# Kernel optimization log

Hardware: AMD Instinct MI355X
Metric: run time of the kernel (lower is better)

## Reference

```python
import jax, jax.numpy as jnp
import numpy as np
from jax import lax

FEAT_STRIDE = 16
PRE_NMS_TOP_N = 6000   # cfg['TEST'].RPN_PRE_NMS_TOP_N
POST_NMS_TOP_N = 300   # cfg['TEST'].RPN_POST_NMS_TOP_N
NMS_THRESH = 0.7       # cfg['TEST'].RPN_NMS_THRESH
MIN_SIZE = 16.0        # cfg['TEST'].RPN_MIN_SIZE
B, A, H, W = 32, 9, 128, 128
NEG_INF = jnp.float32(-1e30)


def _whctrs(a):
    w = a[2] - a[0] + 1.0
    h = a[3] - a[1] + 1.0
    return w, h, a[0] + 0.5 * (w - 1), a[1] + 0.5 * (h - 1)

def _mkanchors(ws, hs, xc, yc):
    ws = ws[:, None]; hs = hs[:, None]
    return np.hstack((xc - 0.5 * (ws - 1), yc - 0.5 * (hs - 1),
                      xc + 0.5 * (ws - 1), yc + 0.5 * (hs - 1)))

def _ratio_enum(anchor, ratios):
    w, h, xc, yc = _whctrs(anchor)
    size = w * h
    ws = np.round(np.sqrt(size / ratios))
    hs = np.round(ws * ratios)
    return _mkanchors(ws, hs, xc, yc)

def _scale_enum(anchor, scales):
    w, h, xc, yc = _whctrs(anchor)
    return _mkanchors(w * scales, h * scales, xc, yc)

def generate_anchors(base_size=16, ratios=np.array([0.5, 1.0, 2.0]), scales=np.array([8.0, 16.0, 32.0])):
    base = np.array([1, 1, base_size, base_size], dtype=np.float64) - 1
    ra = _ratio_enum(base, ratios)
    return np.vstack([_scale_enum(ra[i], scales) for i in range(ra.shape[0])]).astype(np.float32)

_BASE_ANCHORS = generate_anchors()  # (A, 4)

def _all_anchors(h, w):
    sx = np.arange(w) * FEAT_STRIDE
    sy = np.arange(h) * FEAT_STRIDE
    sx, sy = np.meshgrid(sx, sy)  # row-major (h, w) matches permute(0,2,3,1) ordering
    shifts = np.stack([sx.ravel(), sy.ravel(), sx.ravel(), sy.ravel()], axis=1).astype(np.float32)
    return jnp.asarray((shifts[:, None, :] + _BASE_ANCHORS[None, :, :]).reshape(-1, 4))  # (h*w*A, 4)

# ---- bbox_transform_inv / clip_boxes ----

def _decode(anchors, deltas):
    ws = anchors[:, 2] - anchors[:, 0] + 1.0
    hs = anchors[:, 3] - anchors[:, 1] + 1.0
    cx = anchors[:, 0] + 0.5 * ws
    cy = anchors[:, 1] + 0.5 * hs
    dx, dy, dw, dh = deltas[:, 0], deltas[:, 1], deltas[:, 2], deltas[:, 3]
    pcx = dx * ws + cx
    pcy = dy * hs + cy
    pw = jnp.exp(dw) * ws
    ph = jnp.exp(dh) * hs
    return jnp.stack([pcx - 0.5 * pw, pcy - 0.5 * ph, pcx + 0.5 * pw, pcy + 0.5 * ph], axis=1)

def _clip(b, imh, imw):
    x1 = jnp.clip(b[:, 0], 0.0, imw - 1.0)
    y1 = jnp.clip(b[:, 1], 0.0, imh - 1.0)
    x2 = jnp.clip(b[:, 2], 0.0, imw - 1.0)
    y2 = jnp.clip(b[:, 3], 0.0, imh - 1.0)
    return jnp.stack([x1, y1, x2, y2], axis=1)

# ---- greedy NMS: pick top-score box, suppress IoU > thresh, repeat POST times ----

def _nms_select(boxes, scores):
    # boxes: (PRE, 4) score-sorted; scores: (PRE,)
    areas = (boxes[:, 2] - boxes[:, 0] + 1.0) * (boxes[:, 3] - boxes[:, 1] + 1.0)

    def body(i, st):
        s, keep, valid = st
        j = jnp.argmax(s)
        keep = keep.at[i].set(j)
        valid = valid.at[i].set(s[j] > NEG_INF)
        b = boxes[j]
        xx1 = jnp.maximum(b[0], boxes[:, 0])
        yy1 = jnp.maximum(b[1], boxes[:, 1])
        xx2 = jnp.minimum(b[2], boxes[:, 2])
        yy2 = jnp.minimum(b[3], boxes[:, 3])
        inter = jnp.maximum(xx2 - xx1 + 1.0, 0.0) * jnp.maximum(yy2 - yy1 + 1.0, 0.0)
        iou = inter / jnp.maximum(areas[j] + areas - inter, 1e-6)
        s = jnp.where(iou > NMS_THRESH, NEG_INF, s)  # suppresses j itself (IoU = 1)
        return s, keep, valid

    init = (scores, jnp.zeros((POST_NMS_TOP_N,), jnp.int32), jnp.zeros((POST_NMS_TOP_N,), bool))
    _, keep, valid = lax.fori_loop(0, POST_NMS_TOP_N, body, init)
    return keep, valid

def _per_image(sc, dl, info, anchors):
    prop = _clip(_decode(anchors, dl), info[0], info[1])  # (K*A, 4)
    ws = prop[:, 2] - prop[:, 0] + 1.0
    hs = prop[:, 3] - prop[:, 1] + 1.0
    min_sz = MIN_SIZE * info[2]
    sc = jnp.where((ws >= min_sz) & (hs >= min_sz), sc, NEG_INF)
    top_s, top_i = lax.top_k(sc, PRE_NMS_TOP_N)
    cand = prop[top_i]  # (PRE, 4)
    keep, valid = _nms_select(cand, top_s)
    return cand[keep] * valid[:, None].astype(cand.dtype)  # zero-pad invalid rows

def _forward(rpn_cls_prob, rpn_bbox_pred, im_info):
    b, _, h, w = rpn_cls_prob.shape
    anchors = _all_anchors(h, w)
    scores = rpn_cls_prob[:, A:, :, :].transpose(0, 2, 3, 1).reshape(b, -1)  # (b, h*w*A)
    deltas = rpn_bbox_pred.transpose(0, 2, 3, 1).reshape(b, -1, 4)           # (b, h*w*A, 4)
    boxes = jax.vmap(lambda s, d, i: _per_image(s, d, i, anchors))(scores, deltas, im_info)
    ids = jnp.broadcast_to(jnp.arange(b, dtype=boxes.dtype)[:, None, None], (b, POST_NMS_TOP_N, 1))
    return jnp.concatenate([ids, boxes], axis=2)  # (b, POST, 5): [batch_idx, x1, y1, x2, y2]

def setup_inputs() -> dict:
    key = jax.random.key(0)
    k1, k2 = jax.random.split(key)
    rpn_cls_prob = jax.random.uniform(k1, (B, 2 * A, H, W), dtype=jnp.float32)
    rpn_bbox_pred = jax.random.normal(k2, (B, 4 * A, H, W), dtype=jnp.float32) * 0.2
    im_info = jnp.tile(jnp.array([[H * FEAT_STRIDE, W * FEAT_STRIDE, 1.0]], dtype=jnp.float32), (B, 1))
    return {"rpn_cls_prob": rpn_cls_prob, "rpn_bbox_pred": rpn_bbox_pred, "im_info": im_info}

def reference(rpn_cls_prob, rpn_bbox_pred, im_info):
    return _forward(rpn_cls_prob, rpn_bbox_pred, im_info)
```

## Files before the change

### kernel.cpp

```cpp
#include <hip/hip_runtime.h>
#include <cstdint>
#include <cstddef>

#pragma clang fp contract(off)

typedef unsigned long long u64;

#define NB 32
#define NA 9
#define NH 128
#define NW 128
#define HW (NH*NW)
#define NANCH (NA*HW)
#define PRE_N 6000
#define POST_N 300
#define CAND_CAP 8192
#define NMS_T 0.7f
#define GX_GATHER 24
#define NBOX 6144
#define CH 512

__constant__ float c_wa[9] = {184.f,368.f,736.f,128.f,256.f,512.f,88.f,176.f,352.f};
__constant__ float c_ha[9] = {96.f,192.f,384.f,128.f,256.f,512.f,176.f,352.f,704.f};

__device__ __forceinline__ float4 decode_clip(int a, int h, int w,
    float dx, float dy, float dlw, float dlh, float imh, float imw) {
  float wa = c_wa[a], ha = c_ha[a];
  float cx = (float)w * 16.0f + 8.0f;
  float cy = (float)h * 16.0f + 8.0f;
  float pcx = dx * wa + cx;
  float pcy = dy * ha + cy;
  float pw = expf(dlw) * wa;
  float ph = expf(dlh) * ha;
  float x1 = pcx - 0.5f * pw;
  float y1 = pcy - 0.5f * ph;
  float x2 = pcx + 0.5f * pw;
  float y2 = pcy + 0.5f * ph;
  float4 r;
  r.x = fminf(fmaxf(x1, 0.0f), imw - 1.0f);
  r.y = fminf(fmaxf(y1, 0.0f), imh - 1.0f);
  r.z = fminf(fmaxf(x2, 0.0f), imw - 1.0f);
  r.w = fminf(fmaxf(y2, 0.0f), imh - 1.0f);
  return r;
}

__device__ __forceinline__ unsigned score_key(float sc, float bw, float bh, float msz) {
  unsigned bits = __float_as_uint(sc);
  unsigned key = (bits & 0x80000000u) ? ~bits : (bits | 0x80000000u);
  if (!(bw >= msz && bh >= msz)) key = 0u;
  return key;
}

__device__ __forceinline__ bool sup_test4(float4 v, float ar, float4 p, float pa) {
  float xx1 = fmaxf(p.x, v.x), yy1 = fmaxf(p.y, v.y);
  float xx2 = fminf(p.z, v.z), yy2 = fminf(p.w, v.w);
  float iw = fmaxf(xx2 - xx1 + 1.0f, 0.0f);
  float ih = fmaxf(yy2 - yy1 + 1.0f, 0.0f);
  float inter = iw * ih;
  float iou = inter / fmaxf(pa + ar - inter, 1e-6f);
  return iou > NMS_T;
}

__device__ __forceinline__ u64 shfl_xor_u64(u64 x, int m) {
  int lo = __shfl_xor((int)(unsigned)x, m, 64);
  int hi = __shfl_xor((int)(unsigned)(x >> 32), m, 64);
  return ((u64)(unsigned)hi << 32) | (unsigned)lo;
}

__device__ __forceinline__ void reg_step(u64 v[8], int t, int k, int j) {
  #pragma unroll
  for (int r = 0; r < 8; ++r) {
    if ((r & j) == 0) {
      int e = (t << 3) + r;
      bool up = ((e & k) == 0);
      u64 x = v[r], y = v[r | j];
      u64 mx = x > y ? x : y, mn = x > y ? y : x;
      v[r]     = up ? mx : mn;
      v[r | j] = up ? mn : mx;
    }
  }
}

__device__ __forceinline__ void shfl_step(u64 v[8], int t, int k, int j) {
  int m = j >> 3;
  bool lower = ((t & m) == 0);
  #pragma unroll
  for (int r = 0; r < 8; ++r) {
    int e = (t << 3) + r;
    bool up = ((e & k) == 0);
    u64 pv = shfl_xor_u64(v[r], m);
    bool keepmax = (up == lower);
    u64 x = v[r];
    u64 mx = x > pv ? x : pv, mn = x > pv ? pv : x;
    v[r] = keepmax ? mx : mn;
  }
}

__device__ __forceinline__ void lds_step(u64* sm, u64 v[8], int t, int k, int j) {
  int m = j >> 3;
  __syncthreads();
  #pragma unroll
  for (int r = 0; r < 8; ++r) sm[(r << 10) | t] = v[r];
  __syncthreads();
  bool lower = ((t & m) == 0);
  bool up = (((t << 3) & k) == 0);
  bool keepmax = (up == lower);
  int pt = t ^ m;
  #pragma unroll
  for (int r = 0; r < 8; ++r) {
    u64 pv = sm[(r << 10) | pt];
    u64 x = v[r];
    u64 mx = x > pv ? x : pv, mn = x > pv ? pv : x;
    v[r] = keepmax ? mx : mn;
  }
}

__device__ __forceinline__ void p_reg(u64 v[4], int t, int k, int j, bool flip) {
  #pragma unroll
  for (int r = 0; r < 4; ++r) {
    if ((r & j) == 0) {
      int e = (t << 2) + r;
      bool up = (((e & k) == 0) != flip);
      u64 x = v[r], y = v[r | j];
      u64 mx = x > y ? x : y, mn = x > y ? y : x;
      v[r]     = up ? mx : mn;
      v[r | j] = up ? mn : mx;
    }
  }
}

__device__ __forceinline__ void p_shfl(u64 v[4], int t, int k, int j, bool flip) {
  int m = j >> 2;
  bool lower = ((t & m) == 0);
  #pragma unroll
  for (int r = 0; r < 4; ++r) {
    int e = (t << 2) + r;
    bool up = (((e & k) == 0) != flip);
    u64 pv = shfl_xor_u64(v[r], m);
    bool keepmax = (up == lower);
    u64 x = v[r];
    u64 mx = x > pv ? x : pv, mn = x > pv ? pv : x;
    v[r] = keepmax ? mx : mn;
  }
}

__device__ __forceinline__ void p_lds(u64* sm, u64 v[4], int t, int k, int j, bool flip) {
  int m = j >> 2;
  __syncthreads();
  #pragma unroll
  for (int r = 0; r < 4; ++r) sm[(r << 9) | t] = v[r];
  __syncthreads();
  bool lower = ((t & m) == 0);
  bool up = ((((t << 2) & k) == 0) != flip);
  bool keepmax = (up == lower);
  int pt = t ^ m;
  #pragma unroll
  for (int r = 0; r < 4; ++r) {
    u64 pv = sm[(r << 9) | pt];
    u64 x = v[r];
    u64 mx = x > pv ? x : pv, mn = x > pv ? pv : x;
    v[r] = keepmax ? mx : mn;
  }
}

__device__ void find_B(const unsigned* __restrict__ hb, unsigned* part,
                       unsigned* outB, unsigned* outCum) {
  int tid = threadIdx.x;
  unsigned s = 0;
  for (int i = 0; i < 16; ++i) s += hb[tid*16 + i];
  part[tid] = s;
  __syncthreads();
  for (int off = 1; off < 256; off <<= 1) {
    unsigned v = (tid + off < 256) ? part[tid + off] : 0u;
    __syncthreads();
    part[tid] += v;
    __syncthreads();
  }
  unsigned St = part[tid];
  unsigned Sn = (tid < 255) ? part[tid + 1] : 0u;
  if (St >= (unsigned)PRE_N && Sn < (unsigned)PRE_N) {
    unsigned cum = Sn, B = 0, cumAbove = Sn;
    for (int i = 15; i >= 0; --i) {
      unsigned v = hb[tid*16 + i];
      if (cum + v >= (unsigned)PRE_N) { B = (unsigned)(tid*16 + i); cumAbove = cum; break; }
      cum += v;
    }
    *outB = B; *outCum = cumAbove;
  }
  __syncthreads();
}

__device__ void find_thr(const unsigned* __restrict__ hb2, unsigned B, unsigned cum0,
                         unsigned* part, unsigned* outThr) {
  int tid = threadIdx.x;
  unsigned s = 0;
  for (int i = 0; i < 16; ++i) s += hb2[tid*16 + i];
  part[tid] = s;
  __syncthreads();
  for (int off = 1; off < 256; off <<= 1) {
    unsigned v = (tid + off < 256) ? part[tid + off] : 0u;
    __syncthreads();
    part[tid] += v;
    __syncthreads();
  }
  unsigned St = cum0 + part[tid];
  unsigned Sn = cum0 + ((tid < 255) ? part[tid + 1] : 0u);
  if (St >= (unsigned)PRE_N && Sn < (unsigned)PRE_N) {
    unsigned cum = Sn, t = 1u;
    for (int i = 15; i >= 0; --i) {
      unsigned v = hb2[tid*16 + i];
      if (cum + v >= (unsigned)PRE_N) {
        t = (B << 20) | ((unsigned)(tid*16 + i) << 8);
        break;
      }
      cum += v;
    }
    if (t == 0u) t = 1u;
    *outThr = t;
  }
  __syncthreads();
}

__global__ __launch_bounds__(256) void k_keys(const float* __restrict__ cls,
    const float* __restrict__ dl, const float* __restrict__ info,
    unsigned* __restrict__ keys, unsigned* __restrict__ hist) {
  __shared__ unsigned hsh[4096];
  int tid = threadIdx.x;
  for (int i = tid; i < 4096; i += 256) hsh[i] = 0;
  int t = blockIdx.x * 256 + tid;
  int b = blockIdx.y;
  int hw0 = t * 4;
  int h = hw0 >> 7;
  const float* dlb  = dl  + (size_t)b * (4*NA*HW);
  const float* clsb = cls + (size_t)b * (2*NA*HW);
  float imh = info[b*3+0], imw = info[b*3+1];
  float msz = 16.0f * info[b*3+2];
  unsigned* kb = keys + (size_t)b * NANCH;
  __syncthreads();
  #pragma unroll
  for (int a = 0; a < 9; ++a) {
    float4 dx4 = *(const float4*)&dlb[(a*4+0)*HW + hw0];
    float4 dy4 = *(const float4*)&dlb[(a*4+1)*HW + hw0];
    float4 dw4 = *(const float4*)&dlb[(a*4+2)*HW + hw0];
    float4 dh4 = *(const float4*)&dlb[(a*4+3)*HW + hw0];
    float4 sc4 = *(const float4*)&clsb[(NA+a)*HW + hw0];
    uint4 out;
    {
      float4 bx = decode_clip(a, h, (hw0+0)&127, dx4.x, dy4.x, dw4.x, dh4.x, imh, imw);
      out.x = score_key(sc4.x, bx.z-bx.x+1.0f, bx.w-bx.y+1.0f, msz);
    }
    {
      float4 bx = decode_clip(a, h, (hw0+1)&127, dx4.y, dy4.y, dw4.y, dh4.y, imh, imw);
      out.y = score_key(sc4.y, bx.z-bx.x+1.0f, bx.w-bx.y+1.0f, msz);
    }
    {
      float4 bx = decode_clip(a, h, (hw0+2)&127, dx4.z, dy4.z, dw4.z, dh4.z, imh, imw);
      out.z = score_key(sc4.z, bx.z-bx.x+1.0f, bx.w-bx.y+1.0f, msz);
    }
    {
      float4 bx = decode_clip(a, h, (hw0+3)&127, dx4.w, dy4.w, dw4.w, dh4.w, imh, imw);
      out.w = score_key(sc4.w, bx.z-bx.x+1.0f, bx.w-bx.y+1.0f, msz);
    }
    *(uint4*)&kb[a*HW + hw0] = out;
    atomicAdd(&hsh[out.x >> 20], 1u);
    atomicAdd(&hsh[out.y >> 20], 1u);
    atomicAdd(&hsh[out.z >> 20], 1u);
    atomicAdd(&hsh[out.w >> 20], 1u);
  }
  __syncthreads();
  unsigned* gb = hist + ((size_t)b << 12);
  for (int i = tid; i < 4096; i += 256) {
    unsigned v = hsh[i];
    if (v) atomicAdd(&gb[i], v);
  }
}

__global__ __launch_bounds__(256) void k_hist2(const unsigned* __restrict__ keys,
    const unsigned* __restrict__ hist1, unsigned* __restrict__ hist2) {
  __shared__ unsigned h[4096];
  __shared__ unsigned part[256];
  __shared__ unsigned sB, sCum;
  int b = blockIdx.y, tid = threadIdx.x;
  for (int i = tid; i < 4096; i += 256) h[i] = 0;
  __syncthreads();
  find_B(hist1 + ((size_t)b << 12), part, &sB, &sCum);
  unsigned B = sB;
  const unsigned* kb = keys + (size_t)b * NANCH;
  for (int i = blockIdx.x * 256 + tid; i < NANCH; i += gridDim.x * 256) {
    unsigned k = kb[i];
    if ((k >> 20) == B) atomicAdd(&h[(k >> 8) & 4095u], 1u);
  }
  __syncthreads();
  unsigned* gb = hist2 + ((size_t)b << 12);
  for (int i = tid; i < 4096; i += 256) { unsigned v = h[i]; if (v) atomicAdd(&gb[i], v); }
}

__global__ __launch_bounds__(256) void k_gather(const unsigned* __restrict__ keys,
    const unsigned* __restrict__ hist1, const unsigned* __restrict__ hist2,
    const float* __restrict__ dl, const float* __restrict__ info,
    unsigned* __restrict__ cnt, u64* __restrict__ cand,
    float4* __restrict__ boxes) {
  int b = blockIdx.y, tid = threadIdx.x;
  int lane = tid & 63, wv = tid >> 6;
  __shared__ unsigned part[256];
  __shared__ unsigned sB, sCum, sThr;
  __shared__ unsigned wcnt[4], woff[4], blkbase;
  if (tid == 0) sThr = 1u;
  __syncthreads();
  find_B(hist1 + ((size_t)b << 12), part, &sB, &sCum);
  find_thr(hist2 + ((size_t)b << 12), sB, sCum, part, &sThr);
  unsigned t_ = sThr;
  const unsigned* kb = keys + (size_t)b * NANCH;
  const float* dlb = dl + (size_t)b * (4*NA*HW);
  float imh = info[b*3+0], imw = info[b*3+1];
  u64* cb = cand + (size_t)b * CAND_CAP;
  float4* bxc = boxes + (size_t)b * CAND_CAP;
  unsigned* cp = cnt + (size_t)b * 64;
  const int PER_BLK = NANCH / GX_GATHER;
  int base0 = blockIdx.x * PER_BLK;
  for (int it = 0; it < PER_BLK / 256; ++it) {
    int j = base0 + it * 256 + tid;
    unsigned key = kb[j];
    bool pass = key >= t_;
    u64 mask = __ballot(pass);
    if (lane == 0) wcnt[wv] = (unsigned)__popcll(mask);
    __syncthreads();
    if (tid == 0) {
      unsigned s0 = 0;
      for (int w = 0; w < 4; ++w) { woff[w] = s0; s0 += wcnt[w]; }
      blkbase = s0 ? atomicAdd(cp, s0) : 0u;
    }
    __syncthreads();
    if (pass) {
      unsigned pos = blkbase + woff[wv] + (unsigned)__popcll(mask & ((1ull << lane) - 1ull));
      if (pos < CAND_CAP) {
        int a = j >> 14, hw = j & (HW - 1);
        unsigned oi = (unsigned)(hw * 9 + a);
        unsigned noi = (~oi) & 0x3FFFFu;
        cb[pos] = ((u64)key << 32) | ((u64)noi << 13) | (u64)pos;
        bxc[pos] = decode_clip(a, hw >> 7, hw & 127,
                               dlb[(a*4+0)*HW + hw], dlb[(a*4+1)*HW + hw],
                               dlb[(a*4+2)*HW + hw], dlb[(a*4+3)*HW + hw],
                               imh, imw);
      }
    }
    __syncthreads();
  }
}

__global__ __launch_bounds__(512) void k_presort(u64* __restrict__ cand,
                                                 const unsigned* __restrict__ cnt) {
  __shared__ u64 sm[2048];
  int blk = blockIdx.x;
  int b = blk >> 2, q = blk & 3;
  bool flip = (q & 1) != 0;
  unsigned effcnt = cnt[b * 64];
  if (effcnt > CAND_CAP) effcnt = CAND_CAP;
  u64* cb = cand + (size_t)b * CAND_CAP + (size_t)q * 2048;
  int base = q * 2048;
  int t = threadIdx.x;
  int e0 = t << 2;
  u64 v[4];
  #pragma unroll
  for (int r = 0; r < 4; ++r)
    v[r] = ((unsigned)(base + e0 + r) < effcnt) ? cb[e0 + r] : 0ull;
  for (int k = 2; k <= 2048; k <<= 1) {
    int j = k >> 1;
    for (; j >= 256; j >>= 1) p_lds(sm, v, t, k, j, flip);
    for (; j >= 4;   j >>= 1) p_shfl(v, t, k, j, flip);
    for (; j >= 1;   j >>= 1) p_reg(v, t, k, j, flip);
  }
  #pragma unroll
  for (int r = 0; r < 4; ++r) cb[e0 + r] = v[r];
}

__global__ __launch_bounds__(1024) void k_final7(const u64* __restrict__ cand,
    const float4* __restrict__ boxes, float* __restrict__ out) {
  __shared__ float4 bx[NBOX];
  __shared__ float4 cbox2[CH];
  __shared__ float  carea2[CH];
  __shared__ float4 kbox[POST_N];
  __shared__ float  karea[POST_N];
  __shared__ u64 sup[CH][9];
  __shared__ u64 aliveM[8];
  __shared__ u64 kgW[8];
  __shared__ int s_nk;
  u64* sm = (u64*)bx;

  int b = blockIdx.x, tid = threadIdx.x;
  int lane = tid & 63, wv = tid >> 6;
  if (tid == 0) s_nk = 0;

  const u64* cb = cand + (size_t)b * CAND_CAP;
  int e0 = tid << 3;
  u64 v[8];
  #pragma unroll
  for (int r = 0; r < 8; ++r) v[r] = cb[e0 + r];

  for (int k = 4096; k <= CAND_CAP; k <<= 1) {
    int j = k >> 1;
    for (; j >= 512; j >>= 1) lds_step(sm, v, tid, k, j);
    for (; j >= 8;   j >>= 1) shfl_step(v, tid, k, j);
    for (; j >= 1;   j >>= 1) reg_step(v, tid, k, j);
  }
  __syncthreads();

  const float4* bxc = boxes + (size_t)b * CAND_CAP;
  #pragma unroll
  for (int r = 0; r < 8; ++r) {
    int rank = e0 + r;
    if (rank < NBOX) {
      u64 ck = (rank < PRE_N) ? v[r] : 0ull;
      float4 w = make_float4(0.f, 0.f, -1.f, -1.f);
      if ((unsigned)(ck >> 32) != 0u)
        w = bxc[(unsigned)(ck & 0x1FFFu)];
      bx[rank] = w;
    }
  }
  __syncthreads();

  float4 mybx[6];
  float  myar[6];
  int deadm = 0;
  #pragma unroll
  for (int m = 0; m < 6; ++m) {
    float4 w = bx[tid + (m << 10)];
    mybx[m] = w;
    float wid = w.z - w.x + 1.0f;
    myar[m] = wid * (w.w - w.y + 1.0f);
    if (!(wid > 0.0f)) deadm |= (1 << m);
  }

  float* ob = out + (size_t)b * (POST_N * 5);
  int c512 = tid & (CH - 1);
  int seg = tid >> 9;
  bool done = false;

  #pragma unroll
  for (int m = 0; m < 6; ++m) {
    #pragma unroll
    for (int par = 0; par < 2; ++par) {
      if (done) continue;
      int nk0 = s_nk;

      bool own = (tid >> 9) == par;
      int cc = tid - (par << 9);
      bool alive = own && !((deadm >> m) & 1);
      {
        u64 am = __ballot(alive);
        if (own && lane == 0) aliveM[wv & 7] = am;
      }
      __syncthreads();

      int na = 0;
      #pragma unroll
      for (int g = 0; g < 8; ++g) na += (int)__popcll(aliveM[g]);
      if (na == 0) continue;

      if (alive) {
        int cg2 = cc >> 6;
        int pre = 0;
        #pragma unroll
        for (int g = 0; g < 8; ++g) if (g < cg2) pre += (int)__popcll(aliveM[g]);
        pre += (int)__popcll(aliveM[cg2] & ((1ull << (cc & 63)) - 1ull));
        cbox2[pre] = mybx[m];
        carea2[pre] = myar[m];
      }
      __syncthreads();

      {
        int i = c512;
        if (i < na) {
          int ngi = (i >> 6) + 1;
          int gA = seg ? (ngi >> 1) : 0;
          int gB = seg ? ngi : (ngi >> 1);
          if (gA < gB) {
            float4 vi = cbox2[i];
            float ai = carea2[i];
            for (int g = gA; g < gB; ++g) {
              int jmax = i - (g << 6);
              if (jmax > 64) jmax = 64;
              u64 r = 0;
              #pragma unroll 4
              for (int j = 0; j < jmax; ++j) {
                if (sup_test4(vi, ai, cbox2[(g << 6) + j], carea2[(g << 6) + j]))
                  r |= 1ull << j;
              }
              sup[i][g] = r;
            }
          }
        }
      }
      __syncthreads();

      if (tid < 64) {
        u64 kw[8];
        int nst = (na + 63) >> 6;
        u64 srow[8];
        {
          const u64* rp = sup[lane];
          #pragma unroll
          for (int g = 0; g < 8; ++g) srow[g] = rp[g];
        }
        #pragma unroll
        for (int s = 0; s < 8; ++s) {
          u64 nsr[8];
          bool pf = (s + 1 < nst);
          if (pf) {
            const u64* rp = sup[(s + 1) * 64 + lane];
            #pragma unroll
            for (int g = 0; g < 8; ++g) nsr[g] = rp[g];
          }
          u64 kg = 0;
          if (s < nst) {
            int cc2 = s * 64 + lane;
            bool a = (cc2 < na);
            u64 blocked = 0;
            #pragma unroll
            for (int g = 0; g < 8; ++g) if (g < s) blocked |= (srow[g] & kw[g]);
            a = a && (blocked == 0ull);
            u64 r = a ? srow[s] : 0ull;
            u64 cm = __ballot(a);
            while (cm) {
              int j = __builtin_ctzll(cm);
              kg |= 1ull << j;
              u64 rem = __ballot((r >> j) & 1ull);
              cm &= ~(rem | (1ull << j));
            }
          }
          kw[s] = kg;
          if (pf) {
            #pragma unroll
            for (int g = 0; g < 8; ++g) srow[g] = nsr[g];
          }
        }
        if (lane == 0) {
          #pragma unroll
          for (int s = 0; s < 8; ++s) kgW[s] = kw[s];
        }
      }
      __syncthreads();

      if (tid < na) {
        int s = tid >> 6;
        u64 kgw = kgW[s];
        bool kept = (kgw >> (tid & 63)) & 1;
        int pre = 0;
        #pragma unroll
        for (int g = 0; g < 8; ++g) if (g < s) pre += (int)__popcll(kgW[g]);
        pre += (int)__popcll(kgw & ((1ull << (tid & 63)) - 1ull));
        int rank = nk0 + pre;
        if (kept && rank < POST_N) {
          float4 ww = cbox2[tid];
          kbox[rank] = ww; karea[rank] = carea2[tid];
          ob[rank*5+0] = (float)b;
          ob[rank*5+1] = ww.x; ob[rank*5+2] = ww.y; ob[rank*5+3] = ww.z; ob[rank*5+4] = ww.w;
        }
      }
      if (tid == 0) {
        int tot = 0;
        #pragma unroll
        for (int s = 0; s < 8; ++s) tot += (int)__popcll(kgW[s]);
        int nn = nk0 + tot;
        s_nk = nn < POST_N ? nn : POST_N;
      }
      __syncthreads();

      int nk1 = s_nk;
      if (nk1 >= POST_N) { done = true; continue; }
      if (nk1 > nk0) {
        #pragma unroll
        for (int m2 = m; m2 < 6; ++m2) {
          bool fut = (m2 > m) || ((tid >> 9) > par);
          if (fut && !((deadm >> m2) & 1)) {
            for (int k = nk0; k < nk1; ++k) {
              if (sup_test4(mybx[m2], myar[m2], kbox[k], karea[k])) {
                deadm |= (1 << m2);
                break;
              }
            }
          }
        }
      }
    }
  }
  __syncthreads();
  int nk = s_nk;
  for (int r = nk + tid; r < POST_N; r += 1024) {
    ob[r*5+0] = (float)b;
    ob[r*5+1] = 0.f; ob[r*5+2] = 0.f; ob[r*5+3] = 0.f; ob[r*5+4] = 0.f;
  }
}

extern "C" void kernel_launch(void* const* d_in, const int* in_sizes, int n_in,
                              void* d_out, int out_size, void* d_ws, size_t ws_size,
                              hipStream_t stream) {
  const float* cls  = (const float*)d_in[0];
  const float* dl   = (const float*)d_in[1];
  const float* info = (const float*)d_in[2];
  float* out = (float*)d_out;
  char* ws = (char*)d_ws;

  const size_t OFF_KEYS = 0;
  const size_t OFF_H1   = 18874368;
  const size_t OFF_H2   = 19398656;
  const size_t OFF_CNT  = 19922944;
  const size_t OFF_CAND = 19931136;
  const size_t OFF_BOX  = 22028288;
  const size_t WS_NEED  = 26222592;
  if (ws_size < WS_NEED) return;

  unsigned* keys  = (unsigned*)(ws + OFF_KEYS);
  unsigned* h1    = (unsigned*)(ws + OFF_H1);
  unsigned* h2    = (unsigned*)(ws + OFF_H2);
  unsigned* cnt   = (unsigned*)(ws + OFF_CNT);
  u64* cand = (u64*)(ws + OFF_CAND);
  float4* boxes = (float4*)(ws + OFF_BOX);

  hipMemsetAsync(ws + OFF_H1, 0, OFF_CAND - OFF_H1, stream);

  dim3 g1(HW / 1024, NB);
  k_keys<<<g1, 256, 0, stream>>>(cls, dl, info, keys, h1);
  dim3 gh(8, NB);
  k_hist2<<<gh, 256, 0, stream>>>(keys, h1, h2);
  dim3 gg(GX_GATHER, NB);
  k_gather<<<gg, 256, 0, stream>>>(keys, h1, h2, dl, info, cnt, cand, boxes);
  k_presort<<<NB * 4, 512, 0, stream>>>(cand, cnt);
  k_final7<<<NB, 1024, 0, stream>>>(cand, boxes, out);
}
```

Baseline: 315.3 us.

## Presort 4096-element halves and drop kept-box list sync in final NMS

The presort kernel now sorts two 4096-element halves per image (8 elements per thread) instead of four 2048 quarters. This lets the final kernel run only the last merge stage instead of two. The final NMS kernel no longer stores kept boxes into a shared kbox/karea list or keeps a shared counter. Each thread tracks the kept count in a register and tests future candidates directly against the kept bits in the current chunk, which removes one barrier per chunk iteration. The cost is half as many presort blocks, so less parallelism in that stage.

Result: slower. 325.4 us (+3.2%).

```diff
diff --git a/kernel.cpp b/kernel.cpp
--- a/kernel.cpp
+++ b/kernel.cpp
@@ -115,11 +115,11 @@
   }
 }
 
-__device__ __forceinline__ void p_reg(u64 v[4], int t, int k, int j, bool flip) {
-  #pragma unroll
-  for (int r = 0; r < 4; ++r) {
+__device__ __forceinline__ void pf_reg(u64 v[8], int t, int k, int j, bool flip) {
+  #pragma unroll
+  for (int r = 0; r < 8; ++r) {
     if ((r & j) == 0) {
-      int e = (t << 2) + r;
+      int e = (t << 3) + r;
       bool up = (((e & k) == 0) != flip);
       u64 x = v[r], y = v[r | j];
       u64 mx = x > y ? x : y, mn = x > y ? y : x;
@@ -129,12 +129,12 @@
   }
 }
 
-__device__ __forceinline__ void p_shfl(u64 v[4], int t, int k, int j, bool flip) {
-  int m = j >> 2;
+__device__ __forceinline__ void pf_shfl(u64 v[8], int t, int k, int j, bool flip) {
+  int m = j >> 3;
   bool lower = ((t & m) == 0);
   #pragma unroll
-  for (int r = 0; r < 4; ++r) {
-    int e = (t << 2) + r;
+  for (int r = 0; r < 8; ++r) {
+    int e = (t << 3) + r;
     bool up = (((e & k) == 0) != flip);
     u64 pv = shfl_xor_u64(v[r], m);
     bool keepmax = (up == lower);
@@ -144,18 +144,18 @@
   }
 }
 
-__device__ __forceinline__ void p_lds(u64* sm, u64 v[4], int t, int k, int j, bool flip) {
-  int m = j >> 2;
-  __syncthreads();
-  #pragma unroll
-  for (int r = 0; r < 4; ++r) sm[(r << 9) | t] = v[r];
+__device__ __forceinline__ void pf_lds(u64* sm, u64 v[8], int t, int k, int j, bool flip) {
+  int m = j >> 3;
+  __syncthreads();
+  #pragma unroll
+  for (int r = 0; r < 8; ++r) sm[(r << 9) | t] = v[r];
   __syncthreads();
   bool lower = ((t & m) == 0);
-  bool up = ((((t << 2) & k) == 0) != flip);
+  bool up = ((((t << 3) & k) == 0) != flip);
   bool keepmax = (up == lower);
   int pt = t ^ m;
   #pragma unroll
-  for (int r = 0; r < 4; ++r) {
+  for (int r = 0; r < 8; ++r) {
     u64 pv = sm[(r << 9) | pt];
     u64 x = v[r];
     u64 mx = x > pv ? x : pv, mn = x > pv ? pv : x;
@@ -350,46 +350,45 @@
 
 __global__ __launch_bounds__(512) void k_presort(u64* __restrict__ cand,
                                                  const unsigned* __restrict__ cnt) {
-  __shared__ u64 sm[2048];
+  __shared__ u64 sm[4096];
   int blk = blockIdx.x;
-  int b = blk >> 2, q = blk & 3;
-  bool flip = (q & 1) != 0;
+  int b = blk >> 1, q = blk & 1;
+  bool flip = (q != 0);
   unsigned effcnt = cnt[b * 64];
   if (effcnt > CAND_CAP) effcnt = CAND_CAP;
-  u64* cb = cand + (size_t)b * CAND_CAP + (size_t)q * 2048;
-  int base = q * 2048;
+  u64* cb = cand + (size_t)b * CAND_CAP + (size_t)q * 4096;
+  int base = q * 4096;
   int t = threadIdx.x;
-  int e0 = t << 2;
-  u64 v[4];
-  #pragma unroll
-  for (int r = 0; r < 4; ++r)
+  int e0 = t << 3;
+  u64 v[8];
+  #pragma unroll
+  for (int r = 0; r < 8; ++r)
     v[r] = ((unsigned)(base + e0 + r) < effcnt) ? cb[e0 + r] : 0ull;
-  for (int k = 2; k <= 2048; k <<= 1) {
+  for (int k = 2; k <= 8; k <<= 1)
+    for (int j = k >> 1; j >= 1; j >>= 1) pf_reg(v, t, k, j, flip);
+  for (int k = 16; k <= 4096; k <<= 1) {
     int j = k >> 1;
-    for (; j >= 256; j >>= 1) p_lds(sm, v, t, k, j, flip);
-    for (; j >= 4;   j >>= 1) p_shfl(v, t, k, j, flip);
-    for (; j >= 1;   j >>= 1) p_reg(v, t, k, j, flip);
-  }
-  #pragma unroll
-  for (int r = 0; r < 4; ++r) cb[e0 + r] = v[r];
-}
-
-__global__ __launch_bounds__(1024) void k_final7(const u64* __restrict__ cand,
+    for (; j >= 512; j >>= 1) pf_lds(sm, v, t, k, j, flip);
+    for (; j >= 8;   j >>= 1) pf_shfl(v, t, k, j, flip);
+    for (; j >= 1;   j >>= 1) pf_reg(v, t, k, j, flip);
+  }
+  __syncthreads();
+  #pragma unroll
+  for (int r = 0; r < 8; ++r) cb[e0 + r] = v[r];
+}
+
+__global__ __launch_bounds__(1024) void k_final8(const u64* __restrict__ cand,
     const float4* __restrict__ boxes, float* __restrict__ out) {
   __shared__ float4 bx[NBOX];
   __shared__ float4 cbox2[CH];
   __shared__ float  carea2[CH];
-  __shared__ float4 kbox[POST_N];
-  __shared__ float  karea[POST_N];
   __shared__ u64 sup[CH][9];
   __shared__ u64 aliveM[8];
   __shared__ u64 kgW[8];
-  __shared__ int s_nk;
   u64* sm = (u64*)bx;
 
   int b = blockIdx.x, tid = threadIdx.x;
   int lane = tid & 63, wv = tid >> 6;
-  if (tid == 0) s_nk = 0;
 
   const u64* cb = cand + (size_t)b * CAND_CAP;
   int e0 = tid << 3;
@@ -397,7 +396,8 @@
   #pragma unroll
   for (int r = 0; r < 8; ++r) v[r] = cb[e0 + r];
 
-  for (int k = 4096; k <= CAND_CAP; k <<= 1) {
+  {
+    int k = CAND_CAP;
     int j = k >> 1;
     for (; j >= 512; j >>= 1) lds_step(sm, v, tid, k, j);
     for (; j >= 8;   j >>= 1) shfl_step(v, tid, k, j);
@@ -435,13 +435,14 @@
   int c512 = tid & (CH - 1);
   int seg = tid >> 9;
   bool done = false;
+  int nk_reg = 0;
 
   #pragma unroll
   for (int m = 0; m < 6; ++m) {
     #pragma unroll
     for (int par = 0; par < 2; ++par) {
       if (done) continue;
-      int nk0 = s_nk;
+      int nk0 = nk_reg;
 
       bool own = (tid >> 9) == par;
       int cc = tid - (par << 9);
@@ -552,40 +553,42 @@
         int rank = nk0 + pre;
         if (kept && rank < POST_N) {
           float4 ww = cbox2[tid];
-          kbox[rank] = ww; karea[rank] = carea2[tid];
           ob[rank*5+0] = (float)b;
           ob[rank*5+1] = ww.x; ob[rank*5+2] = ww.y; ob[rank*5+3] = ww.z; ob[rank*5+4] = ww.w;
         }
       }
-      if (tid == 0) {
-        int tot = 0;
-        #pragma unroll
-        for (int s = 0; s < 8; ++s) tot += (int)__popcll(kgW[s]);
-        int nn = nk0 + tot;
-        s_nk = nn < POST_N ? nn : POST_N;
-      }
-      __syncthreads();
-
-      int nk1 = s_nk;
-      if (nk1 >= POST_N) { done = true; continue; }
-      if (nk1 > nk0) {
+
+      int tot = 0;
+      #pragma unroll
+      for (int s = 0; s < 8; ++s) tot += (int)__popcll(kgW[s]);
+      int nn = nk0 + tot;
+      nk_reg = nn < POST_N ? nn : POST_N;
+      if (nk_reg >= POST_N) { done = true; continue; }
+      if (tot > 0) {
         #pragma unroll
         for (int m2 = m; m2 < 6; ++m2) {
           bool fut = (m2 > m) || ((tid >> 9) > par);
           if (fut && !((deadm >> m2) & 1)) {
-            for (int k = nk0; k < nk1; ++k) {
-              if (sup_test4(mybx[m2], myar[m2], kbox[k], karea[k])) {
-                deadm |= (1 << m2);
-                break;
+            bool dead = false;
+            #pragma unroll
+            for (int s = 0; s < 8; ++s) {
+              u64 kg = kgW[s];
+              while (kg && !dead) {
+                int j = __builtin_ctzll(kg);
+                kg &= kg - 1;
+                int col = (s << 6) + j;
+                if (sup_test4(mybx[m2], myar[m2], cbox2[col], carea2[col]))
+                  dead = true;
               }
             }
+            if (dead) deadm |= (1 << m2);
           }
         }
       }
     }
   }
   __syncthreads();
-  int nk = s_nk;
+  int nk = nk_reg;
   for (int r = nk + tid; r < POST_N; r += 1024) {
     ob[r*5+0] = (float)b;
     ob[r*5+1] = 0.f; ob[r*5+2] = 0.f; ob[r*5+3] = 0.f; ob[r*5+4] = 0.f;
@@ -625,6 +628,6 @@
   k_hist2<<<gh, 256, 0, stream>>>(keys, h1, h2);
   dim3 gg(GX_GATHER, NB);
   k_gather<<<gg, 256, 0, stream>>>(keys, h1, h2, dl, info, cnt, cand, boxes);
-  k_presort<<<NB * 4, 512, 0, stream>>>(cand, cnt);
-  k_final7<<<NB, 1024, 0, stream>>>(cand, boxes, out);
-}
+  k_presort<<<NB * 2, 512, 0, stream>>>(cand, cnt);
+  k_final8<<<NB, 1024, 0, stream>>>(cand, boxes, out);
+}
```
